# Performance work log

Hardware: AMD Instinct MI355X
Metric: run time of the kernel (lower is better)

The kernel has to match this reference:

```python
import jax, jax.numpy as jnp
import numpy as np


def setup_inputs() -> dict:
    key = jax.random.key(0)
    k1, k2, k3, k4 = jax.random.split(key, 4)
    B, S, D, Hd = 4, 4096, 1024, 128
    x = jax.random.normal(k1, (B, S, D), dtype=jnp.float32)
    # nn.Linear(D, Hd, bias=False) weight has shape [Hd, D]; we store transposed [D, Hd]
    scale = 1.0 / np.sqrt(D)
    Wq = jax.random.normal(k2, (D, Hd), dtype=jnp.float32) * scale
    Wk = jax.random.normal(k3, (D, Hd), dtype=jnp.float32) * scale
    Wv = jax.random.normal(k4, (D, Hd), dtype=jnp.float32) * scale
    return {"x": x, "Wq": Wq, "Wk": Wk, "Wv": Wv}


def reference(x, Wq, Wk, Wv):
    # Q/K/V projections: [B,S,D] @ [D,Hd] -> [B,S,Hd]
    Q = jnp.einsum("bsd,dh->bsh", x, Wq)
    K = jnp.einsum("bsd,dh->bsh", x, Wk)
    V = jnp.einsum("bsd,dh->bsh", x, Wv)
    head_dim = K.shape[-1]
    inv_sqrt = jnp.asarray(1.0 / np.sqrt(head_dim), dtype=Q.dtype)
    # full [B,S,S] scores (matches the original non-fused implementation)
    scores = jnp.einsum("bqh,bkh->bqk", Q, K) * inv_sqrt
    attn = jax.nn.softmax(scores, axis=-1)
    out = jnp.einsum("bqk,bkh->bqh", attn, V)
    return out
```

## Files before the change

kernel.cpp:

```cpp
#include <hip/hip_runtime.h>


#define BB 4
#define SS 4096
#define DD 1024
#define HDIM 128
#define NTIL 16
#define KVB 64

typedef _Float16 f16;
typedef _Float16 half8 __attribute__((ext_vector_type(8)));
typedef _Float16 half4 __attribute__((ext_vector_type(4)));
typedef __fp16 fp16x2 __attribute__((ext_vector_type(2)));
typedef float f32x4 __attribute__((ext_vector_type(4)));

__device__ __forceinline__ void gload_lds16(const void* g, void* l) {
  __builtin_amdgcn_global_load_lds(
      (const __attribute__((address_space(1))) void*)g,
      (__attribute__((address_space(3))) void*)l, 16, 0, 0);
}

__device__ __forceinline__ f32x4 mfma16(half8 a, half8 b, f32x4 c) {
  return __builtin_amdgcn_mfma_f32_16x16x32_f16(a, b, c, 0, 0, 0);
}

__global__ void wt_kernel(const float* __restrict__ Wq, const float* __restrict__ Wk,
                          const float* __restrict__ Wv, f16* __restrict__ w3t) {
  const int n = blockIdx.x;
  const float* W = (n < 128) ? Wq : (n < 256) ? Wk : Wv;
  const int col = n & 127;
  for (int d = threadIdx.x; d < DD; d += blockDim.x)
    w3t[(size_t)n * DD + d] = (f16)W[(size_t)d * HDIM + col];
}

__global__ __launch_bounds__(256)
__attribute__((amdgpu_waves_per_eu(1, 1)))
void proj_kernel(
    const float* __restrict__ x, const f16* __restrict__ w3t,
    f16* __restrict__ Qm, f16* __restrict__ Km, f16* __restrict__ VTm) {
  __shared__ __align__(16) float xa[2][64 * 32];
  const int tid = threadIdx.x;
  const int lane = tid & 63;
  const int wid = tid >> 6;
  const int lo = lane & 15, hi = lane >> 4;
  const int row0 = blockIdx.x * 64;

  auto STAGE = [&](int kc, int bufsel) {
#pragma unroll
    for (int i = 0; i < 2; ++i) {
      const int cid = i * 256 + tid;
      const int r = cid >> 3, c4 = cid & 7;
      gload_lds16((const char*)(x + (size_t)(row0 + r) * DD + kc * 32) +
                      ((c4 * 16) ^ ((r & 7) << 4)),
                  (char*)&xa[bufsel][0] + (size_t)(i * 256 + wid * 64) * 16);
    }
  };

  half8 bfA[6], bfB[6];
  auto BLOAD = [&](half8 (&bf)[6], int kc) {
#pragma unroll
    for (int nf = 0; nf < 6; ++nf) {
      const int n = wid * 96 + nf * 16 + lo;
      bf[nf] = *(const half8*)(w3t + (size_t)n * DD + kc * 32 + hi * 8);
    }
  };

  f32x4 acc[4][6];
#pragma unroll
  for (int m = 0; m < 4; ++m)
#pragma unroll
    for (int nf = 0; nf < 6; ++nf) acc[m][nf] = (f32x4){0.f, 0.f, 0.f, 0.f};

  auto ITER = [&](int kc, int cur, half8 (&bfCur)[6], half8 (&bfNext)[6]) {
    if (kc + 1 < 32) {
      STAGE(kc + 1, cur ^ 1);
      asm volatile("s_waitcnt vmcnt(8)" ::: "memory");
    } else {
      asm volatile("s_waitcnt vmcnt(6)" ::: "memory");
    }
    __builtin_amdgcn_s_barrier();

    if (kc + 1 < 32) BLOAD(bfNext, kc + 1);
    __builtin_amdgcn_sched_barrier(0);

    const char* xb = (const char*)&xa[cur][0];
    half8 af[4];
#pragma unroll
    for (int m = 0; m < 4; ++m) {
      const int row = m * 16 + lo;
      const int base = row * 128 + hi * 32;
      const int swz = (row & 7) << 4;
      f32x4 a0 = *(const f32x4*)(xb + (base ^ swz));
      f32x4 a1 = *(const f32x4*)(xb + ((base + 16) ^ swz));
      union { fp16x2 h2[4]; half8 h8; } u;
      u.h2[0] = __builtin_amdgcn_cvt_pkrtz(a0[0], a0[1]);
      u.h2[1] = __builtin_amdgcn_cvt_pkrtz(a0[2], a0[3]);
      u.h2[2] = __builtin_amdgcn_cvt_pkrtz(a1[0], a1[1]);
      u.h2[3] = __builtin_amdgcn_cvt_pkrtz(a1[2], a1[3]);
      af[m] = u.h8;
    }
#pragma unroll
    for (int nf = 0; nf < 6; ++nf)
#pragma unroll
      for (int m = 0; m < 4; ++m)
        acc[m][nf] = mfma16(af[m], bfCur[nf], acc[m][nf]);

    __builtin_amdgcn_s_barrier();
  };

  STAGE(0, 0);
  BLOAD(bfA, 0);
#pragma unroll 1
  for (int kc = 0; kc < 32; kc += 2) {
    ITER(kc, 0, bfA, bfB);
    ITER(kc + 1, 1, bfB, bfA);
  }

#pragma unroll
  for (int m = 0; m < 4; ++m) {
#pragma unroll
    for (int nf = 0; nf < 6; ++nf) {
      const int n = wid * 96 + nf * 16 + lo;
#pragma unroll
      for (int r = 0; r < 4; ++r) {
        const int row = row0 + m * 16 + hi * 4 + r;
        const f16 v = (f16)acc[m][nf][r];
        if (n < 128) {
          Qm[(size_t)row * HDIM + n] = v;
        } else if (n < 256) {
          Km[(size_t)row * HDIM + (n - 128)] = v;
        } else {
          const int b = row >> 12, s = row & 4095;
          const int t = s & 31;
          const int sp = (s & ~31) | ((t & 0x0C) << 1) | ((t & 0x10) >> 2) | (t & 3);
          VTm[((size_t)b * HDIM + (n - 256)) * SS + sp] = v;
        }
      }
    }
  }
}

__global__ __launch_bounds__(512)
__attribute__((amdgpu_waves_per_eu(2, 2)))
void attn_kernel(
    const f16* __restrict__ Qm, const f16* __restrict__ Km,
    const f16* __restrict__ VTm, float* __restrict__ out,
    float* __restrict__ lws) {
  __shared__ __align__(16) f16 Kt[2][KVB * 128];
  __shared__ __align__(16) f16 Vt[2][128 * KVB];

  const int xcd = blockIdx.x & 7;
  const int idx = blockIdx.x >> 3;
  const int group = xcd * 2 + (idx >> 4);
  const int b = group >> 2;
  const int split = group & 3;
  const int qt = idx & 15;
  const int tid = threadIdx.x;
  const int wid = tid >> 6;
  const int lane = tid & 63;
  const int lo = lane & 15, hi = lane >> 4;
  const int q0 = qt * 256 + wid * 32;
  const int kbase = split * (NTIL * KVB);

  constexpr float SCL2E = 0.12751744560817508f;

  half8 qf[2][4];
#pragma unroll
  for (int m = 0; m < 2; ++m)
#pragma unroll
    for (int c = 0; c < 4; ++c) {
      half8 q = *(const half8*)(Qm + (size_t)(b * SS + q0 + m * 16 + lo) * HDIM +
                                c * 32 + hi * 8);
#pragma unroll
      for (int j = 0; j < 8; ++j) q[j] = (f16)((float)q[j] * SCL2E);
      qf[m][c] = q;
    }

  f32x4 of[2][8];
#pragma unroll
  for (int m = 0; m < 2; ++m)
#pragma unroll
    for (int g2 = 0; g2 < 8; ++g2) of[m][g2] = (f32x4){0.f, 0.f, 0.f, 0.f};
  float lrun[2] = {0.f, 0.f};

  const char* kgb = (const char*)(Km + ((size_t)b * SS + kbase) * HDIM);
  const char* vgb = (const char*)(VTm + (size_t)b * HDIM * SS) + (size_t)kbase * 2;

  auto STAGE = [&](int kt2, int bufsel) {
    char* kd = (char*)&Kt[bufsel][0];
    char* vd = (char*)&Vt[bufsel][0];
#pragma unroll
    for (int i = 0; i < 2; ++i) {
      const int cid = i * 512 + tid;
      const int r = cid >> 4, c4 = cid & 15;
      gload_lds16(kgb + (size_t)(kt2 * KVB + r) * 256 + ((c4 * 16) ^ ((r & 7) << 4)),
                  kd + (size_t)(i * 512 + wid * 64) * 16);
    }
#pragma unroll
    for (int i = 0; i < 2; ++i) {
      const int cid = i * 512 + tid;
      const int r = cid >> 3, c8 = cid & 7;
      gload_lds16(vgb + (size_t)r * (SS * 2) + (size_t)(kt2 * KVB) * 2 +
                      ((c8 * 16) ^ ((r & 7) << 4)),
                  vd + (size_t)(i * 512 + wid * 64) * 16);
    }
  };

  STAGE(0, 0);
  int cur = 0;
#pragma unroll 1
  for (int kt = 0; kt < NTIL; ++kt) {
    if (kt + 1 < NTIL) {
      STAGE(kt + 1, cur ^ 1);
      asm volatile("s_waitcnt vmcnt(4)" ::: "memory");
    } else {
      asm volatile("s_waitcnt vmcnt(0)" ::: "memory");
    }
    __builtin_amdgcn_s_barrier();

    const char* KtC = (const char*)&Kt[cur][0];
    const char* VtC = (const char*)&Vt[cur][0];

    f32x4 sc[2][4];
#pragma unroll
    for (int m = 0; m < 2; ++m)
#pragma unroll
      for (int g = 0; g < 4; ++g) sc[m][g] = (f32x4){0.f, 0.f, 0.f, 0.f};
#pragma unroll
    for (int c = 0; c < 4; ++c)
#pragma unroll
      for (int g = 0; g < 4; ++g) {
        const int row = g * 16 + lo;
        const half8 kb = *(const half8*)(KtC + row * 256 +
                                         ((c * 64 + hi * 16) ^ ((row & 7) << 4)));
        sc[0][g] = mfma16(kb, qf[0][c], sc[0][g]);
        sc[1][g] = mfma16(kb, qf[1][c], sc[1][g]);
      }

    half8 pa[2][2];
#pragma unroll
    for (int m = 0; m < 2; ++m) {
#pragma unroll
      for (int kc = 0; kc < 2; ++kc) {
        union { half4 h4[2]; half8 h8; } pu;
#pragma unroll
        for (int gg = 0; gg < 2; ++gg) {
          const int g = kc * 2 + gg;
          const float p0 = __builtin_amdgcn_exp2f(sc[m][g][0]);
          const float p1 = __builtin_amdgcn_exp2f(sc[m][g][1]);
          const float p2 = __builtin_amdgcn_exp2f(sc[m][g][2]);
          const float p3 = __builtin_amdgcn_exp2f(sc[m][g][3]);
          union { fp16x2 h2[2]; half4 h4; } u;
          u.h2[0] = __builtin_amdgcn_cvt_pkrtz(p0, p1);
          u.h2[1] = __builtin_amdgcn_cvt_pkrtz(p2, p3);
          pu.h4[gg] = u.h4;
          lrun[m] += (p0 + p1) + (p2 + p3);
        }
        pa[m][kc] = pu.h8;
      }
    }

#pragma unroll
    for (int kc = 0; kc < 2; ++kc)
#pragma unroll
      for (int g2 = 0; g2 < 8; ++g2) {
        const int row = g2 * 16 + lo;
        const half8 vb = *(const half8*)(VtC + row * 128 +
                                         ((kc * 64 + hi * 16) ^ ((row & 7) << 4)));
        of[0][g2] = mfma16(pa[0][kc], vb, of[0][g2]);
        of[1][g2] = mfma16(pa[1][kc], vb, of[1][g2]);
      }

    __builtin_amdgcn_s_barrier();
    cur ^= 1;
  }

#pragma unroll
  for (int m = 0; m < 2; ++m) {
    lrun[m] += __shfl_xor(lrun[m], 16, 64);
    lrun[m] += __shfl_xor(lrun[m], 32, 64);
  }

  float* op = out + ((size_t)(b * SS + q0)) * HDIM;
#pragma unroll
  for (int m = 0; m < 2; ++m) {
#pragma unroll
    for (int r = 0; r < 4; ++r) {
      const int row = m * 16 + hi * 4 + r;
#pragma unroll
      for (int g2 = 0; g2 < 8; ++g2)
        atomicAdd(&op[(size_t)row * HDIM + g2 * 16 + lo], of[m][g2][r]);
    }
  }
  if (hi == 0) {
    atomicAdd(&lws[b * SS + q0 + lo], lrun[0]);
    atomicAdd(&lws[b * SS + q0 + 16 + lo], lrun[1]);
  }
}

__global__ void norm_kernel(float* __restrict__ out, const float* __restrict__ lws) {
  const int idx = blockIdx.x * 256 + threadIdx.x;
  f32x4 v = ((const f32x4*)out)[idx];
  const float inv = 1.0f / lws[idx >> 5];
  v[0] *= inv; v[1] *= inv; v[2] *= inv; v[3] *= inv;
  ((f32x4*)out)[idx] = v;
}

extern "C" void kernel_launch(void* const* d_in, const int* in_sizes, int n_in,
                              void* d_out, int out_size, void* d_ws, size_t ws_size,
                              hipStream_t stream) {
  (void)in_sizes; (void)n_in; (void)out_size; (void)ws_size;
  const float* x  = (const float*)d_in[0];
  const float* Wq = (const float*)d_in[1];
  const float* Wk = (const float*)d_in[2];
  const float* Wv = (const float*)d_in[3];
  float* out = (float*)d_out;

  f16* Qm  = (f16*)d_ws;
  f16* Km  = Qm + (size_t)BB * SS * HDIM;
  f16* VTm = Km + (size_t)BB * SS * HDIM;
  f16* W3  = VTm + (size_t)BB * SS * HDIM;
  float* lws = (float*)(W3 + (size_t)384 * DD);

  hipMemsetAsync(out, 0, (size_t)BB * SS * HDIM * sizeof(float), stream);
  hipMemsetAsync(lws, 0, (size_t)BB * SS * sizeof(float), stream);

  hipLaunchKernelGGL(wt_kernel, dim3(384), dim3(256), 0, stream, Wq, Wk, Wv, W3);
  hipLaunchKernelGGL(proj_kernel, dim3(256), dim3(256), 0, stream, x, W3, Qm, Km, VTm);
  hipLaunchKernelGGL(attn_kernel, dim3(256), dim3(512), 0, stream, Qm, Km, VTm, out, lws);
  hipLaunchKernelGGL(norm_kernel, dim3(2048), dim3(256), 0, stream, out, lws);
}
```

Measured before the change: 119.6 us.

## Triple-buffer LDS staging in projection and attention kernels, remap attention block ids

Both the projection and attention kernels go from double to triple buffering, so global-to-LDS loads run two tiles ahead with the waitcnt thresholds adjusted to match. The projection weight fragments also rotate through three register sets. The attention block-to-(batch, qtile, split) mapping changes so each XCD handles one batch half, which is meant to improve L2 locality of K/V. The cost is more LDS and registers, which may hurt occupancy or spill.

```diff
diff --git a/kernel.cpp b/kernel.cpp
--- a/kernel.cpp
+++ b/kernel.cpp
@@ -38,7 +38,7 @@
 void proj_kernel(
     const float* __restrict__ x, const f16* __restrict__ w3t,
     f16* __restrict__ Qm, f16* __restrict__ Km, f16* __restrict__ VTm) {
-  __shared__ __align__(16) float xa[2][64 * 32];
+  __shared__ __align__(16) float xa[3][64 * 32];
   const int tid = threadIdx.x;
   const int lane = tid & 63;
   const int wid = tid >> 6;
@@ -56,7 +56,7 @@
     }
   };
 
-  half8 bfA[6], bfB[6];
+  half8 bf0[6], bf1[6], bf2[6];
   auto BLOAD = [&](half8 (&bf)[6], int kc) {
 #pragma unroll
     for (int nf = 0; nf < 6; ++nf) {
@@ -71,19 +71,21 @@
 #pragma unroll
     for (int nf = 0; nf < 6; ++nf) acc[m][nf] = (f32x4){0.f, 0.f, 0.f, 0.f};
 
-  auto ITER = [&](int kc, int cur, half8 (&bfCur)[6], half8 (&bfNext)[6]) {
-    if (kc + 1 < 32) {
-      STAGE(kc + 1, cur ^ 1);
-      asm volatile("s_waitcnt vmcnt(8)" ::: "memory");
+  auto ITER = [&](int kc, int xcb, int xnb, half8 (&bfCur)[6], half8 (&bfN2)[6]) {
+    if (kc + 2 < 32) {
+      STAGE(kc + 2, xnb);
+      asm volatile("s_waitcnt vmcnt(16)" ::: "memory");
+    } else if (kc + 1 < 32) {
+      asm volatile("s_waitcnt vmcnt(14)" ::: "memory");
     } else {
       asm volatile("s_waitcnt vmcnt(6)" ::: "memory");
     }
     __builtin_amdgcn_s_barrier();
 
-    if (kc + 1 < 32) BLOAD(bfNext, kc + 1);
+    if (kc + 2 < 32) BLOAD(bfN2, kc + 2);
     __builtin_amdgcn_sched_barrier(0);
 
-    const char* xb = (const char*)&xa[cur][0];
+    const char* xb = (const char*)&xa[xcb][0];
     half8 af[4];
 #pragma unroll
     for (int m = 0; m < 4; ++m) {
@@ -109,12 +111,18 @@
   };
 
   STAGE(0, 0);
-  BLOAD(bfA, 0);
+  STAGE(1, 1);
+  BLOAD(bf0, 0);
+  BLOAD(bf1, 1);
 #pragma unroll 1
-  for (int kc = 0; kc < 32; kc += 2) {
-    ITER(kc, 0, bfA, bfB);
-    ITER(kc + 1, 1, bfB, bfA);
-  }
+  for (int g = 0; g < 10; ++g) {
+    const int kc = g * 3;
+    ITER(kc + 0, 0, 2, bf0, bf2);
+    ITER(kc + 1, 1, 0, bf1, bf0);
+    ITER(kc + 2, 2, 1, bf2, bf1);
+  }
+  ITER(30, 0, 2, bf0, bf2);
+  ITER(31, 1, 0, bf1, bf0);
 
 #pragma unroll
   for (int m = 0; m < 4; ++m) {
@@ -146,15 +154,14 @@
     const f16* __restrict__ Qm, const f16* __restrict__ Km,
     const f16* __restrict__ VTm, float* __restrict__ out,
     float* __restrict__ lws) {
-  __shared__ __align__(16) f16 Kt[2][KVB * 128];
-  __shared__ __align__(16) f16 Vt[2][128 * KVB];
+  __shared__ __align__(16) f16 Kt[3][KVB * 128];
+  __shared__ __align__(16) f16 Vt[3][128 * KVB];
 
   const int xcd = blockIdx.x & 7;
-  const int idx = blockIdx.x >> 3;
-  const int group = xcd * 2 + (idx >> 4);
-  const int b = group >> 2;
-  const int split = group & 3;
-  const int qt = idx & 15;
+  const int i = blockIdx.x >> 3;
+  const int b = xcd >> 1;
+  const int qt = (i & 7) * 2 + (xcd & 1);
+  const int split = i >> 3;
   const int tid = threadIdx.x;
   const int wid = tid >> 6;
   const int lane = tid & 63;
@@ -190,36 +197,35 @@
     char* kd = (char*)&Kt[bufsel][0];
     char* vd = (char*)&Vt[bufsel][0];
 #pragma unroll
-    for (int i = 0; i < 2; ++i) {
-      const int cid = i * 512 + tid;
+    for (int i2 = 0; i2 < 2; ++i2) {
+      const int cid = i2 * 512 + tid;
       const int r = cid >> 4, c4 = cid & 15;
       gload_lds16(kgb + (size_t)(kt2 * KVB + r) * 256 + ((c4 * 16) ^ ((r & 7) << 4)),
-                  kd + (size_t)(i * 512 + wid * 64) * 16);
-    }
-#pragma unroll
-    for (int i = 0; i < 2; ++i) {
-      const int cid = i * 512 + tid;
+                  kd + (size_t)(i2 * 512 + wid * 64) * 16);
+    }
+#pragma unroll
+    for (int i2 = 0; i2 < 2; ++i2) {
+      const int cid = i2 * 512 + tid;
       const int r = cid >> 3, c8 = cid & 7;
       gload_lds16(vgb + (size_t)r * (SS * 2) + (size_t)(kt2 * KVB) * 2 +
                       ((c8 * 16) ^ ((r & 7) << 4)),
-                  vd + (size_t)(i * 512 + wid * 64) * 16);
-    }
-  };
-
-  STAGE(0, 0);
-  int cur = 0;
-#pragma unroll 1
-  for (int kt = 0; kt < NTIL; ++kt) {
-    if (kt + 1 < NTIL) {
-      STAGE(kt + 1, cur ^ 1);
+                  vd + (size_t)(i2 * 512 + wid * 64) * 16);
+    }
+  };
+
+  auto ITER = [&](int kt, int cb, int nb) {
+    if (kt + 2 < NTIL) {
+      STAGE(kt + 2, nb);
+      asm volatile("s_waitcnt vmcnt(8)" ::: "memory");
+    } else if (kt + 1 < NTIL) {
       asm volatile("s_waitcnt vmcnt(4)" ::: "memory");
     } else {
       asm volatile("s_waitcnt vmcnt(0)" ::: "memory");
     }
     __builtin_amdgcn_s_barrier();
 
-    const char* KtC = (const char*)&Kt[cur][0];
-    const char* VtC = (const char*)&Vt[cur][0];
+    const char* KtC = (const char*)&Kt[cb][0];
+    const char* VtC = (const char*)&Vt[cb][0];
 
     f32x4 sc[2][4];
 #pragma unroll
@@ -272,8 +278,18 @@
       }
 
     __builtin_amdgcn_s_barrier();
-    cur ^= 1;
-  }
+  };
+
+  STAGE(0, 0);
+  STAGE(1, 1);
+#pragma unroll 1
+  for (int g = 0; g < 5; ++g) {
+    const int kt = g * 3;
+    ITER(kt + 0, 0, 2);
+    ITER(kt + 1, 1, 0);
+    ITER(kt + 2, 2, 1);
+  }
+  ITER(15, 0, 2);
 
 #pragma unroll
   for (int m = 0; m < 2; ++m) {
```

After: 112.6 us, median of 2. -5.8%, faster.
